# Kernel optimization log

Hardware: AMD Instinct MI355X
Metric: run time of the kernel (lower is better)

## Reference

```python
import jax, jax.numpy as jnp
import numpy as np


def setup_inputs() -> dict:
    key = jax.random.key(0)
    ks = jax.random.split(key, 6)
    B, N, d = 8, 2048, 64
    h = jax.random.normal(ks[0], (B, N, d), dtype=jnp.float32)
    adj = jax.random.randint(ks[1], (B, N, N), 0, 2, dtype=jnp.int32)
    h_root = jax.random.normal(ks[2], (B, N), dtype=jnp.float32)
    weight = jax.random.normal(ks[3], (d, d), dtype=jnp.float32) * (1.0 / np.sqrt(d))
    a1 = jax.random.normal(ks[4], (d, 1), dtype=jnp.float32) * (1.0 / np.sqrt(d))
    a2 = jax.random.normal(ks[5], (d, 1), dtype=jnp.float32) * (1.0 / np.sqrt(d))
    return {"h": h, "adj": adj, "h_root": h_root, "weight": weight, "a1": a1, "a2": a2}


def reference(h, adj, h_root, weight, a1, a2):
    h0 = h
    hw = jax.nn.relu(jnp.matmul(h, weight))          # (B,N,d)
    t1 = jnp.matmul(hw, a1)                          # (B,N,1)
    t2 = jnp.matmul(hw, a2)                          # (B,N,1)
    # e[b,i,j] = relu(t1[b,i] + t2[b,j])  (broadcast, same as repeat/view in torch)
    e = jax.nn.relu(t1 + jnp.swapaxes(t2, -1, -2))   # (B,N,N)
    # FAITHFUL to source bug: pos0 = -9e15 * zeros_like(adj) == 0, so
    # non-edges get logit 0 (not -inf) before softmax.
    e = jnp.where(adj > 0, e, jnp.zeros_like(e))
    attention = jax.nn.softmax(e, axis=-1)           # (B,N,N)
    embedding = jnp.matmul(attention, hw)            # (B,N,d)
    # assign = h_root[:,:,None] @ ones(B,1,d) -> h_root broadcast over d;
    # assign > 0  <=>  h_root > 0 since ones are positive.
    assign = h_root[:, :, None] * jnp.ones((1, 1, hw.shape[-1]), dtype=hw.dtype)
    embedding = jnp.where(assign > 0, embedding, h0)
    return embedding
```

## Files before the change

### kernel.cpp

```cpp
#include <hip/hip_runtime.h>
#include <hip/hip_bf16.h>

#define BATCH 8
#define NN    2048
#define DD    64
#define BN    (BATCH * NN)

#define JSPAN  (NN / 4)
#define KSTEPS (JSPAN / 32)

typedef __attribute__((ext_vector_type(8))) short bf16x8;
typedef __attribute__((ext_vector_type(4))) float f32x4;

static __device__ __forceinline__ unsigned f2bf_pk(float lo, float hi) {
  unsigned ul = __float_as_uint(lo);
  unsigned uh = __float_as_uint(hi);
  ul = (ul + 0x7fffu + ((ul >> 16) & 1u)) >> 16;
  uh = (uh + 0x7fffu + ((uh >> 16) & 1u)) & 0xffff0000u;
  return ul | uh;
}

__global__ __launch_bounds__(256) void k1_hw_t1_t2(
    const float* __restrict__ h, const float* __restrict__ W,
    const float* __restrict__ a1, const float* __restrict__ a2,
    unsigned short* __restrict__ hwT, float* __restrict__ t1, float* __restrict__ t2) {
  __shared__ float ht[64 * 36];
  __shared__ float Ws[64 * 64];
  __shared__ unsigned short bt[64 * 40];

  const int t  = threadIdx.x;
  const int r0 = blockIdx.x * 32;

#pragma unroll
  for (int r = 0; r < 4; ++r) {
    int f = t + 256 * r;
    reinterpret_cast<float4*>(Ws)[f] = reinterpret_cast<const float4*>(W)[f];
  }
#pragma unroll
  for (int r = 0; r < 2; ++r) {
    int f = t + 256 * r;
    int i = f >> 4, j4 = f & 15;
    float4 v = reinterpret_cast<const float4*>(h + (size_t)(r0 + i) * DD)[j4];
    ht[(4 * j4 + 0) * 36 + i] = v.x;
    ht[(4 * j4 + 1) * 36 + i] = v.y;
    ht[(4 * j4 + 2) * 36 + i] = v.z;
    ht[(4 * j4 + 3) * 36 + i] = v.w;
  }
  __syncthreads();

  const int trow = t >> 4, kcol = t & 15;
  float4 acc0 = make_float4(0.f, 0.f, 0.f, 0.f);
  float4 acc1 = make_float4(0.f, 0.f, 0.f, 0.f);

#pragma unroll 8
  for (int j = 0; j < 64; ++j) {
    float2 hv = *reinterpret_cast<const float2*>(&ht[j * 36 + 2 * trow]);
    float4 wv = reinterpret_cast<const float4*>(Ws)[j * 16 + kcol];
    acc0.x = fmaf(hv.x, wv.x, acc0.x); acc0.y = fmaf(hv.x, wv.y, acc0.y);
    acc0.z = fmaf(hv.x, wv.z, acc0.z); acc0.w = fmaf(hv.x, wv.w, acc0.w);
    acc1.x = fmaf(hv.y, wv.x, acc1.x); acc1.y = fmaf(hv.y, wv.y, acc1.y);
    acc1.z = fmaf(hv.y, wv.z, acc1.z); acc1.w = fmaf(hv.y, wv.w, acc1.w);
  }

  acc0.x = fmaxf(acc0.x, 0.f); acc0.y = fmaxf(acc0.y, 0.f);
  acc0.z = fmaxf(acc0.z, 0.f); acc0.w = fmaxf(acc0.w, 0.f);
  acc1.x = fmaxf(acc1.x, 0.f); acc1.y = fmaxf(acc1.y, 0.f);
  acc1.z = fmaxf(acc1.z, 0.f); acc1.w = fmaxf(acc1.w, 0.f);

  float4 a1v = reinterpret_cast<const float4*>(a1)[kcol];
  float4 a2v = reinterpret_cast<const float4*>(a2)[kcol];
  float s1_0 = acc0.x * a1v.x + acc0.y * a1v.y + acc0.z * a1v.z + acc0.w * a1v.w;
  float s1_1 = acc1.x * a1v.x + acc1.y * a1v.y + acc1.z * a1v.z + acc1.w * a1v.w;
  float s2_0 = acc0.x * a2v.x + acc0.y * a2v.y + acc0.z * a2v.z + acc0.w * a2v.w;
  float s2_1 = acc1.x * a2v.x + acc1.y * a2v.y + acc1.z * a2v.z + acc1.w * a2v.w;
#pragma unroll
  for (int m = 1; m <= 8; m <<= 1) {
    s1_0 += __shfl_xor(s1_0, m, 64);
    s1_1 += __shfl_xor(s1_1, m, 64);
    s2_0 += __shfl_xor(s2_0, m, 64);
    s2_1 += __shfl_xor(s2_1, m, 64);
  }
  {
    int row = r0 + 2 * trow;
    if (kcol == 0) {
      t1[row] = s1_0; t1[row + 1] = s1_1;
      t2[row] = s2_0; t2[row + 1] = s2_1;
    }
  }

  {
    const float* a0 = &acc0.x;
    const float* a1p = &acc1.x;
#pragma unroll
    for (int c = 0; c < 4; ++c) {
      int k = 4 * kcol + c;
      *reinterpret_cast<unsigned*>(&bt[k * 40 + 2 * trow]) = f2bf_pk(a0[c], a1p[c]);
    }
  }
  __syncthreads();
  {
    int k = t >> 2, jp = t & 3;
    int bb = r0 >> 11;
    int jb = r0 & (NN - 1);
    *reinterpret_cast<int4*>(hwT + ((size_t)bb * DD + k) * NN + jb + jp * 8) =
        *reinterpret_cast<const int4*>(&bt[k * 40 + jp * 8]);
  }
}

__global__ __launch_bounds__(256, 4) void k2_attn(
    const unsigned short* __restrict__ hwT, const int* __restrict__ adj,
    const float* __restrict__ t1, const float* __restrict__ t2,
    const float* __restrict__ h, const float* __restrict__ h_root,
    float* __restrict__ out) {
  __shared__ float t2s[NN];
  __shared__ float os[4][16][68];
  __shared__ float denos[4][16];

  const int t    = threadIdx.x;
  const int b    = blockIdx.x >> 7;
  const int i0   = (blockIdx.x & 127) * 16;
  const int w    = t >> 6;
  const int lane = t & 63;
  const int m    = lane & 15;
  const int quad = lane >> 4;
  const int jbase = w * JSPAN;

#pragma unroll
  for (int r = 0; r < 2; ++r)
    reinterpret_cast<float4*>(t2s)[t + 256 * r] =
        reinterpret_cast<const float4*>(t2 + b * NN)[t + 256 * r];

  const int rowbase = b * NN + i0;
  const float t1v = t1[rowbase + m];
  const bool  act = h_root[rowbase + m] > 0.f;
  const int* adjl = adj + (size_t)(rowbase + m) * NN + jbase + quad * 8;
  const unsigned short* hwp = hwT + (size_t)b * DD * NN + jbase + quad * 8 + m * NN;

  f32x4 acc[4];
#pragma unroll
  for (int g = 0; g < 4; ++g) acc[g] = (f32x4){0.f, 0.f, 0.f, 0.f};
  float den = 0.f;

  int4 c0 = make_int4(0,0,0,0), c1 = c0, n10 = c0, n11 = c0, n20, n21;
  if (act) {
    c0  = *reinterpret_cast<const int4*>(adjl);
    c1  = *reinterpret_cast<const int4*>(adjl + 4);
    n10 = *reinterpret_cast<const int4*>(adjl + 32);
    n11 = *reinterpret_cast<const int4*>(adjl + 36);
  }

  __syncthreads();

#pragma unroll 1
  for (int ks = 0; ks < KSTEPS; ++ks) {
    n20 = make_int4(0,0,0,0); n21 = n20;
    if (ks + 2 < KSTEPS && act) {
      const int* ap = adjl + (ks + 2) * 32;
      n20 = *reinterpret_cast<const int4*>(ap);
      n21 = *reinterpret_cast<const int4*>(ap + 4);
    }

    bf16x8 B0 = *reinterpret_cast<const bf16x8*>(hwp + 0 * 16 * NN + ks * 32);
    bf16x8 B1 = *reinterpret_cast<const bf16x8*>(hwp + 1 * 16 * NN + ks * 32);
    bf16x8 B2 = *reinterpret_cast<const bf16x8*>(hwp + 2 * 16 * NN + ks * 32);
    bf16x8 B3 = *reinterpret_cast<const bf16x8*>(hwp + 3 * 16 * NN + ks * 32);

    const float* t2p = &t2s[jbase + ks * 32 + quad * 8];
    float4 e0 = *reinterpret_cast<const float4*>(t2p);
    float4 e1 = *reinterpret_cast<const float4*>(t2p + 4);

    float p0 = (c0.x > 0) ? __expf(fmaxf(t1v + e0.x, 0.f)) : 1.f;
    float p1 = (c0.y > 0) ? __expf(fmaxf(t1v + e0.y, 0.f)) : 1.f;
    float p2 = (c0.z > 0) ? __expf(fmaxf(t1v + e0.z, 0.f)) : 1.f;
    float p3 = (c0.w > 0) ? __expf(fmaxf(t1v + e0.w, 0.f)) : 1.f;
    float p4 = (c1.x > 0) ? __expf(fmaxf(t1v + e1.x, 0.f)) : 1.f;
    float p5 = (c1.y > 0) ? __expf(fmaxf(t1v + e1.y, 0.f)) : 1.f;
    float p6 = (c1.z > 0) ? __expf(fmaxf(t1v + e1.z, 0.f)) : 1.f;
    float p7 = (c1.w > 0) ? __expf(fmaxf(t1v + e1.w, 0.f)) : 1.f;
    den += ((p0 + p1) + (p2 + p3)) + ((p4 + p5) + (p6 + p7));

    union { bf16x8 v; unsigned u[4]; } Af;
    Af.u[0] = f2bf_pk(p0, p1); Af.u[1] = f2bf_pk(p2, p3);
    Af.u[2] = f2bf_pk(p4, p5); Af.u[3] = f2bf_pk(p6, p7);

    acc[0] = __builtin_amdgcn_mfma_f32_16x16x32_bf16(Af.v, B0, acc[0], 0, 0, 0);
    acc[1] = __builtin_amdgcn_mfma_f32_16x16x32_bf16(Af.v, B1, acc[1], 0, 0, 0);
    acc[2] = __builtin_amdgcn_mfma_f32_16x16x32_bf16(Af.v, B2, acc[2], 0, 0, 0);
    acc[3] = __builtin_amdgcn_mfma_f32_16x16x32_bf16(Af.v, B3, acc[3], 0, 0, 0);

    c0 = n10; c1 = n11; n10 = n20; n11 = n21;
  }

  den += __shfl_xor(den, 16, 64);
  den += __shfl_xor(den, 32, 64);
  if (quad == 0) denos[w][m] = den;

#pragma unroll
  for (int g = 0; g < 4; ++g)
#pragma unroll
    for (int r = 0; r < 4; ++r)
      os[w][quad * 4 + r][g * 16 + m] = acc[g][r];
  __syncthreads();

  {
    const int i = t >> 4, k4 = t & 15;
    float4 a = make_float4(0.f, 0.f, 0.f, 0.f);
    float d = 0.f;
#pragma unroll
    for (int ww = 0; ww < 4; ++ww) {
      float4 p = *reinterpret_cast<const float4*>(&os[ww][i][k4 * 4]);
      a.x += p.x; a.y += p.y; a.z += p.z; a.w += p.w;
      d += denos[ww][i];
    }
    const size_t row = (size_t)rowbase + i;
    float4 res;
    if (h_root[row] > 0.f) {
      const float inv = 1.f / d;
      res.x = a.x * inv; res.y = a.y * inv; res.z = a.z * inv; res.w = a.w * inv;
    } else {
      res = reinterpret_cast<const float4*>(h + row * DD)[k4];
    }
    reinterpret_cast<float4*>(out + row * DD)[k4] = res;
  }
}

extern "C" void kernel_launch(void* const* d_in, const int* in_sizes, int n_in,
                              void* d_out, int out_size, void* d_ws, size_t ws_size,
                              hipStream_t stream) {
  const float* h      = (const float*)d_in[0];
  const int*   adj    = (const int*)d_in[1];
  const float* h_root = (const float*)d_in[2];
  const float* W      = (const float*)d_in[3];
  const float* a1     = (const float*)d_in[4];
  const float* a2     = (const float*)d_in[5];
  float* out = (float*)d_out;

  unsigned short* hwT = (unsigned short*)d_ws;
  float* t1 = (float*)(hwT + (size_t)BN * DD);
  float* t2 = t1 + BN;

  k1_hw_t1_t2<<<BN / 32, 256, 0, stream>>>(h, W, a1, a2, hwT, t1, t2);
  k2_attn<<<BATCH * (NN / 16), 256, 0, stream>>>(hwT, adj, t1, t2, h, h_root, out);
}
```

Before: 225.0 us.

## Compress adjacency rows to LDS bitmasks and pre-tile hwT for MFMA loads

Each wave now reads adjacency rows with fully coalesced per-lane loads, reduces them to bitmasks via ballot, and stores the masks in shared memory. The attention loop then reads a 32-bit mask word per step instead of strided int4 loads. k1 also writes hwT in an MFMA-fragment-tiled layout so each lane's B loads are contiguous 16-byte chunks. This targets the poorly coalesced adjacency stream, which dominates traffic. In exchange it adds a serial mask-building prologue per block with no overlap with compute.

```diff
diff --git a/kernel.cpp b/kernel.cpp
--- a/kernel.cpp
+++ b/kernel.cpp
@@ -5,9 +5,7 @@
 #define NN    2048
 #define DD    64
 #define BN    (BATCH * NN)
-
-#define JSPAN  (NN / 4)
-#define KSTEPS (JSPAN / 32)
+#define MWORDS 66
 
 typedef __attribute__((ext_vector_type(8))) short bf16x8;
 typedef __attribute__((ext_vector_type(4))) float f32x4;
@@ -74,11 +72,11 @@
   float s2_0 = acc0.x * a2v.x + acc0.y * a2v.y + acc0.z * a2v.z + acc0.w * a2v.w;
   float s2_1 = acc1.x * a2v.x + acc1.y * a2v.y + acc1.z * a2v.z + acc1.w * a2v.w;
 #pragma unroll
-  for (int m = 1; m <= 8; m <<= 1) {
-    s1_0 += __shfl_xor(s1_0, m, 64);
-    s1_1 += __shfl_xor(s1_1, m, 64);
-    s2_0 += __shfl_xor(s2_0, m, 64);
-    s2_1 += __shfl_xor(s2_1, m, 64);
+  for (int mm = 1; mm <= 8; mm <<= 1) {
+    s1_0 += __shfl_xor(s1_0, mm, 64);
+    s1_1 += __shfl_xor(s1_1, mm, 64);
+    s2_0 += __shfl_xor(s2_0, mm, 64);
+    s2_1 += __shfl_xor(s2_1, mm, 64);
   }
   {
     int row = r0 + 2 * trow;
@@ -100,10 +98,12 @@
   __syncthreads();
   {
     int k = t >> 2, jp = t & 3;
+    int g = k >> 4, n = k & 15;
     int bb = r0 >> 11;
     int jb = r0 & (NN - 1);
-    *reinterpret_cast<int4*>(hwT + ((size_t)bb * DD + k) * NN + jb + jp * 8) =
-        *reinterpret_cast<const int4*>(&bt[k * 40 + jp * 8]);
+    int ks = jb >> 5;
+    size_t base = ((((size_t)bb * (NN / 32) + ks) * 4 + g) * 64 + (jp * 16 + n)) * 8;
+    *reinterpret_cast<int4*>(hwT + base) = *reinterpret_cast<const int4*>(&bt[k * 40 + jp * 8]);
   }
 }
 
@@ -112,6 +112,7 @@
     const float* __restrict__ t1, const float* __restrict__ t2,
     const float* __restrict__ h, const float* __restrict__ h_root,
     float* __restrict__ out) {
+  __shared__ unsigned maskS[16 * MWORDS];
   __shared__ float t2s[NN];
   __shared__ float os[4][16][68];
   __shared__ float denos[4][16];
@@ -123,7 +124,6 @@
   const int lane = t & 63;
   const int m    = lane & 15;
   const int quad = lane >> 4;
-  const int jbase = w * JSPAN;
 
 #pragma unroll
   for (int r = 0; r < 2; ++r)
@@ -131,52 +131,68 @@
         reinterpret_cast<const float4*>(t2 + b * NN)[t + 256 * r];
 
   const int rowbase = b * NN + i0;
+
+#pragma unroll 1
+  for (int rr = 0; rr < 4; ++rr) {
+    const int row = w * 4 + rr;
+    const bool active = h_root[rowbase + row] > 0.f;
+    if (active) {
+      const int* ap = adj + (size_t)(rowbase + row) * NN + lane;
+#pragma unroll 1
+      for (int sb = 0; sb < 2; ++sb) {
+        int v[16];
+#pragma unroll
+        for (int s = 0; s < 16; ++s) v[s] = ap[(sb * 16 + s) * 64];
+#pragma unroll
+        for (int s = 0; s < 16; ++s) {
+          unsigned long long bal = __ballot(v[s] > 0);
+          if (lane == 0)
+            *reinterpret_cast<unsigned long long*>(
+                &maskS[row * MWORDS + (sb * 16 + s) * 2]) = bal;
+        }
+      }
+    } else {
+      maskS[row * MWORDS + lane] = 0u;
+    }
+  }
+  __syncthreads();
+
   const float t1v = t1[rowbase + m];
-  const bool  act = h_root[rowbase + m] > 0.f;
-  const int* adjl = adj + (size_t)(rowbase + m) * NN + jbase + quad * 8;
-  const unsigned short* hwp = hwT + (size_t)b * DD * NN + jbase + quad * 8 + m * NN;
+  const int ks0 = w * 16;
 
   f32x4 acc[4];
 #pragma unroll
   for (int g = 0; g < 4; ++g) acc[g] = (f32x4){0.f, 0.f, 0.f, 0.f};
   float den = 0.f;
 
-  int4 c0 = make_int4(0,0,0,0), c1 = c0, n10 = c0, n11 = c0, n20, n21;
-  if (act) {
-    c0  = *reinterpret_cast<const int4*>(adjl);
-    c1  = *reinterpret_cast<const int4*>(adjl + 4);
-    n10 = *reinterpret_cast<const int4*>(adjl + 32);
-    n11 = *reinterpret_cast<const int4*>(adjl + 36);
-  }
-
-  __syncthreads();
+  unsigned mcur = maskS[m * MWORDS + ks0];
 
 #pragma unroll 1
-  for (int ks = 0; ks < KSTEPS; ++ks) {
-    n20 = make_int4(0,0,0,0); n21 = n20;
-    if (ks + 2 < KSTEPS && act) {
-      const int* ap = adjl + (ks + 2) * 32;
-      n20 = *reinterpret_cast<const int4*>(ap);
-      n21 = *reinterpret_cast<const int4*>(ap + 4);
-    }
-
-    bf16x8 B0 = *reinterpret_cast<const bf16x8*>(hwp + 0 * 16 * NN + ks * 32);
-    bf16x8 B1 = *reinterpret_cast<const bf16x8*>(hwp + 1 * 16 * NN + ks * 32);
-    bf16x8 B2 = *reinterpret_cast<const bf16x8*>(hwp + 2 * 16 * NN + ks * 32);
-    bf16x8 B3 = *reinterpret_cast<const bf16x8*>(hwp + 3 * 16 * NN + ks * 32);
-
-    const float* t2p = &t2s[jbase + ks * 32 + quad * 8];
+  for (int kk = 0; kk < 16; ++kk) {
+    const int ks = ks0 + kk;
+    unsigned mnext = 0;
+    if (kk + 1 < 16) mnext = maskS[m * MWORDS + ks + 1];
+
+    const unsigned short* bp =
+        hwT + ((((size_t)b * (NN / 32) + ks) * 4) * 64 + lane) * 8;
+    bf16x8 B0 = *reinterpret_cast<const bf16x8*>(bp);
+    bf16x8 B1 = *reinterpret_cast<const bf16x8*>(bp + 512);
+    bf16x8 B2 = *reinterpret_cast<const bf16x8*>(bp + 1024);
+    bf16x8 B3 = *reinterpret_cast<const bf16x8*>(bp + 1536);
+
+    const float* t2p = &t2s[ks * 32 + quad * 8];
     float4 e0 = *reinterpret_cast<const float4*>(t2p);
     float4 e1 = *reinterpret_cast<const float4*>(t2p + 4);
 
-    float p0 = (c0.x > 0) ? __expf(fmaxf(t1v + e0.x, 0.f)) : 1.f;
-    float p1 = (c0.y > 0) ? __expf(fmaxf(t1v + e0.y, 0.f)) : 1.f;
-    float p2 = (c0.z > 0) ? __expf(fmaxf(t1v + e0.z, 0.f)) : 1.f;
-    float p3 = (c0.w > 0) ? __expf(fmaxf(t1v + e0.w, 0.f)) : 1.f;
-    float p4 = (c1.x > 0) ? __expf(fmaxf(t1v + e1.x, 0.f)) : 1.f;
-    float p5 = (c1.y > 0) ? __expf(fmaxf(t1v + e1.y, 0.f)) : 1.f;
-    float p6 = (c1.z > 0) ? __expf(fmaxf(t1v + e1.z, 0.f)) : 1.f;
-    float p7 = (c1.w > 0) ? __expf(fmaxf(t1v + e1.w, 0.f)) : 1.f;
+    const unsigned mm8 = mcur >> (quad * 8);
+    float p0 = (mm8 & 1u)   ? __expf(fmaxf(t1v + e0.x, 0.f)) : 1.f;
+    float p1 = (mm8 & 2u)   ? __expf(fmaxf(t1v + e0.y, 0.f)) : 1.f;
+    float p2 = (mm8 & 4u)   ? __expf(fmaxf(t1v + e0.z, 0.f)) : 1.f;
+    float p3 = (mm8 & 8u)   ? __expf(fmaxf(t1v + e0.w, 0.f)) : 1.f;
+    float p4 = (mm8 & 16u)  ? __expf(fmaxf(t1v + e1.x, 0.f)) : 1.f;
+    float p5 = (mm8 & 32u)  ? __expf(fmaxf(t1v + e1.y, 0.f)) : 1.f;
+    float p6 = (mm8 & 64u)  ? __expf(fmaxf(t1v + e1.z, 0.f)) : 1.f;
+    float p7 = (mm8 & 128u) ? __expf(fmaxf(t1v + e1.w, 0.f)) : 1.f;
     den += ((p0 + p1) + (p2 + p3)) + ((p4 + p5) + (p6 + p7));
 
     union { bf16x8 v; unsigned u[4]; } Af;
@@ -188,7 +204,7 @@
     acc[2] = __builtin_amdgcn_mfma_f32_16x16x32_bf16(Af.v, B2, acc[2], 0, 0, 0);
     acc[3] = __builtin_amdgcn_mfma_f32_16x16x32_bf16(Af.v, B3, acc[3], 0, 0, 0);
 
-    c0 = n10; c1 = n11; n10 = n20; n11 = n21;
+    mcur = mnext;
   }
 
   den += __shfl_xor(den, 16, 64);
```

Result: faster. 210.2 us (-6.6%).
